# Performance work log

Measured on AMD Instinct MI355X. Metric: run time of the kernel, lower is better.

Reference implementation:

```python
import jax, jax.numpy as jnp
import numpy as np

B, N, F = 32, 1024, 32
EPS = 1e-5


def _bn(h):
    # torch BatchNorm1d(x.size(1)) applied to [B, N, C]: normalizes each node index
    # over (batch, channel) axes, training mode, biased variance, weight=1, bias=0.
    m = h.mean(axis=(0, 2), keepdims=True)
    v = h.var(axis=(0, 2), keepdims=True)
    return (h - m) / jnp.sqrt(v + EPS)


def setup_inputs() -> dict:
    key = jax.random.key(0)
    ks = jax.random.split(key, 16)
    x = jax.random.normal(ks[0], (B, N, F), dtype=jnp.float32)
    adj = jax.random.uniform(ks[1], (B, N, N), dtype=jnp.float32)

    def w(k, i, o):
        return jax.random.normal(k, (i, o), dtype=jnp.float32) * (1.0 / np.sqrt(i))

    inp = {
        'x': x, 'adj': adj,
        'W1': w(ks[2], F, 4), 'b1': jnp.zeros((4,), jnp.float32),
        'W2': w(ks[3], 4, 2), 'b2': jnp.zeros((2,), jnp.float32),
        'W3': w(ks[4], 6, 4), 'b3': jnp.zeros((4,), jnp.float32),
        'W5': w(ks[5], 6, 4), 'b5': jnp.zeros((4,), jnp.float32),
        'W7': w(ks[6], 6, 4), 'b7': jnp.zeros((4,), jnp.float32),
        'Wl': w(ks[7], 24, 3), 'bl': jnp.zeros((3,), jnp.float32),
    }
    return inp


def reference(x, adj, W1, b1, W2, b2, W3, b3, W5, b5, W7, b7, Wl, bl):
    n = adj.shape[-1]
    # DenseGCNConv normalization (identical for every conv call): set diag to 1,
    # then D^{-1/2} A D^{-1/2} with degree clamped at 1. Precompute once.
    diag = jnp.eye(n, dtype=bool)
    A = jnp.where(diag, jnp.asarray(1.0, adj.dtype), adj)  # [B,N,N]
    d = jnp.clip(A.sum(-1), 1.0, None) ** -0.5              # [B,N]
    A = d[:, :, None] * A * d[:, None, :]

    def gcn(h, W, b):
        return jnp.matmul(A, jnp.matmul(h, W)) + b

    def block(h, Wa, ba):
        x1 = _bn(jax.nn.relu(gcn(h, Wa, ba)))      # [B,N,4]
        x2 = _bn(jax.nn.relu(gcn(x1, W2, b2)))     # [B,N,2] (conv2 reused)
        x12 = jnp.concatenate([x1, x2], axis=-1)   # [B,N,6]
        return x12, x12.max(axis=1)                # pooled [B,6]

    h, p1 = block(x, W1, b1)
    h, p2 = block(h, W3, b3)
    h, p3 = block(h, W5, b5)
    h, p4 = block(h, W7, b7)
    out = jnp.concatenate([p1, p2, p3, p4], axis=-1)  # [B,24]
    ypred = out @ Wl + bl                             # [B,3]
    return ypred
```

## Files before the change

### kernel.cpp

```cpp
#include <hip/hip_runtime.h>
#include <hip/hip_fp16.h>

#define NB 32
#define NN 1024

typedef _Float16 h2 __attribute__((ext_vector_type(2)));
typedef _Float16 h8 __attribute__((ext_vector_type(8)));

static const size_t F_D     = 0;
static const size_t F_STATS = 32768;
static const size_t F_XW1   = 49152;
static constexpr size_t F_Y[8] = {180224, 311296, 376832, 507904,
                                  573440, 704512, 770048, 901120};
static const size_t AH_BYTE_OFF  = 3866624;
static const size_t WS_NEED_HALF = AH_BYTE_OFF + (size_t)NB*NN*NN*2;

__device__ __forceinline__ float fdot2f(h2 a, h2 b, float c) {
#if __has_builtin(__builtin_amdgcn_fdot2)
    return __builtin_amdgcn_fdot2(a, b, c, false);
#else
    return c + (float)a[0]*(float)b[0] + (float)a[1]*(float)b[1];
#endif
}

__global__ __launch_bounds__(256)
void k0_prep(const float* __restrict__ adj, const float* __restrict__ x,
             const float* __restrict__ W1, float* __restrict__ dd,
             float* __restrict__ xw1, float* __restrict__ stats,
             __half* __restrict__ ahw)
{
    const int tid = threadIdx.x;
    const int bx  = blockIdx.x;
    if (bx < 8192) {
        const int lane = tid & 63, wid = tid >> 6;
        const int row = bx * 4 + wid;
        const int n = row & (NN - 1);
        const float4* arow = (const float4*)(adj + (size_t)row * NN);
        uint2* hrow = (uint2*)(ahw + (size_t)row * NN);
        float s = 0.f;
        #pragma unroll
        for (int it = 0; it < 4; ++it) {
            const int idx = lane + it * 64;
            float4 v = arow[idx];
            const int k0 = idx * 4;
            v.x = (k0 + 0 == n) ? 1.f : v.x;
            v.y = (k0 + 1 == n) ? 1.f : v.y;
            v.z = (k0 + 2 == n) ? 1.f : v.z;
            v.w = (k0 + 3 == n) ? 1.f : v.w;
            s += v.x + v.y + v.z + v.w;
            if (ahw) {
                __half2 h01 = __floats2half2_rn(v.x, v.y);
                __half2 h23 = __floats2half2_rn(v.z, v.w);
                uint2 u;
                u.x = *(unsigned*)&h01; u.y = *(unsigned*)&h23;
                hrow[idx] = u;
            }
        }
        #pragma unroll
        for (int m = 1; m < 64; m <<= 1) s += __shfl_xor(s, m);
        if (lane == 0) dd[row] = rsqrtf(fmaxf(s, 1.f));
    } else if (bx < 8320) {
        const int id = (bx - 8192) * 256 + tid;
        const float4* xr = (const float4*)(x + (size_t)id * 32);
        float in[32];
        #pragma unroll
        for (int i = 0; i < 8; ++i) {
            float4 v = xr[i];
            in[4*i]=v.x; in[4*i+1]=v.y; in[4*i+2]=v.z; in[4*i+3]=v.w;
        }
        float o[4] = {0.f,0.f,0.f,0.f};
        #pragma unroll
        for (int i = 0; i < 32; ++i)
            #pragma unroll
            for (int c = 0; c < 4; ++c) o[c] += in[i] * W1[i*4+c];
        *(float4*)(xw1 + (size_t)id * 4) = make_float4(o[0],o[1],o[2],o[3]);
    } else {
        const int id = (bx - 8320) * 256 + tid;
        stats[id] = 0.f;
    }
}

__device__ __forceinline__ void stage_chunk(const __half* __restrict__ ah,
        int rowbase, int wid, int lane, int ck, char* sbuf)
{
    #pragma unroll
    for (int i = 0; i < 4; ++i) {
        const int ob = (wid << 12) + (i << 10);
        const int o  = ob + (lane << 4);
        const int row = o >> 9;
        const int scol = (o & 511) ^ ((row & 7) << 4);
        const char* g = (const char*)ah +
            (((size_t)(rowbase + row)) * NN + (size_t)ck * 256) * 2 + scol;
#if __has_builtin(__builtin_amdgcn_global_load_lds)
        __builtin_amdgcn_global_load_lds(
            (const __attribute__((address_space(1))) void*)g,
            (__attribute__((address_space(3))) void*)(sbuf + ob),
            16, 0, 0);
#else
        *(float4*)(sbuf + o) = *(const float4*)g;
#endif
    }
}

template<int CIN1, int CIN2, int COUT>
__global__ __launch_bounds__(512, 4)
void pass_half(const __half* __restrict__ ah, const float* __restrict__ dd,
               const float* __restrict__ xw1,
               const float* __restrict__ src1, const float* __restrict__ st1,
               const float* __restrict__ src2, const float* __restrict__ st2,
               const float* __restrict__ W, const float* __restrict__ bias,
               float* __restrict__ Y, float* __restrict__ stout)
{
    __shared__ char sA[2][32768];
    __shared__ _Float16 XPh[COUT][1280];
    const int tid = threadIdx.x, lane = tid & 63, wid = tid >> 6;
    const int b    = blockIdx.x >> 4;
    const int tile = (blockIdx.x & 15) << 6;
    const int rowbase = b * NN + tile;

    stage_chunk(ah, rowbase, wid, lane, 0, sA[0]);

    for (int k = tid; k < NN; k += 512) {
        float xw[COUT];
        if constexpr (CIN1 == 0) {
            const float4 v = *(const float4*)(xw1 + ((size_t)b*NN + k) * 4);
            xw[0]=v.x; xw[1]=v.y; xw[2]=v.z; xw[3]=v.w;
        } else {
            float in[CIN1 + CIN2];
            {
                const float cnt = 1.f / (32.f * CIN1);
                const float m  = st1[k] * cnt;
                const float ms = st1[NN + k] * cnt;
                const float iv = rsqrtf(ms - m*m + 1e-5f);
                const float4 v = *(const float4*)(src1 + ((size_t)b*NN + k) * CIN1);
                in[0]=(v.x-m)*iv; in[1]=(v.y-m)*iv; in[2]=(v.z-m)*iv; in[3]=(v.w-m)*iv;
            }
            if constexpr (CIN2 > 0) {
                const float cnt = 1.f / (32.f * CIN2);
                const float m  = st2[k] * cnt;
                const float ms = st2[NN + k] * cnt;
                const float iv = rsqrtf(ms - m*m + 1e-5f);
                const float2 v = *(const float2*)(src2 + ((size_t)b*NN + k) * CIN2);
                in[CIN1+0]=(v.x-m)*iv; in[CIN1+1]=(v.y-m)*iv;
            }
            #pragma unroll
            for (int c = 0; c < COUT; ++c) {
                float s = 0.f;
                #pragma unroll
                for (int i = 0; i < CIN1+CIN2; ++i) s += in[i]*W[i*COUT+c];
                xw[c] = s;
            }
        }
        const float dk = dd[b*NN + k];
        const int mk = k + ((k>>5)<<3);
        #pragma unroll
        for (int c = 0; c < COUT; ++c) XPh[c][mk] = (_Float16)(xw[c]*dk);
    }
    asm volatile("s_waitcnt vmcnt(0)" ::: "memory");
    __syncthreads();

    const int rj = lane >> 3, ll = lane & 7;
    const int trow = (wid << 3) + rj;
    float acc[COUT];
    #pragma unroll
    for (int c = 0; c < COUT; ++c) acc[c] = 0.f;

    int buf = 0;
    for (int ck = 0; ck < 4; ++ck) {
        if (ck < 3) stage_chunk(ah, rowbase, wid, lane, ck+1, sA[buf^1]);
        const char* aB = &sA[buf][trow << 9];
        #pragma unroll
        for (int sub = 0; sub < 4; ++sub) {
            const h8 av = *(const h8*)(aB + (((((ll<<2)+sub)) ^ rj) << 4));
            const int k = ck*256 + ll*32 + sub*8;
            const int mk = k + ((k>>5)<<3);
            #pragma unroll
            for (int c = 0; c < COUT; ++c) {
                const h8 xv = *(const h8*)&XPh[c][mk];
                float s = acc[c];
                s = fdot2f(h2{av[0],av[1]}, h2{xv[0],xv[1]}, s);
                s = fdot2f(h2{av[2],av[3]}, h2{xv[2],xv[3]}, s);
                s = fdot2f(h2{av[4],av[5]}, h2{xv[4],xv[5]}, s);
                s = fdot2f(h2{av[6],av[7]}, h2{xv[6],xv[7]}, s);
                acc[c] = s;
            }
        }
        asm volatile("s_waitcnt vmcnt(0)" ::: "memory");
        __syncthreads();
        buf ^= 1;
    }

    #pragma unroll
    for (int c = 0; c < COUT; ++c) {
        float v = acc[c];
        v += __shfl_xor(v, 1); v += __shfl_xor(v, 2); v += __shfl_xor(v, 4);
        acc[c] = v;
    }
    if (ll == 0) {
        const int n = tile + trow;
        const float dn = dd[b*NN + n];
        float s = 0.f, q2 = 0.f;
        float y[COUT];
        #pragma unroll
        for (int c = 0; c < COUT; ++c) {
            float t = acc[c] * dn + bias[c];
            t = fmaxf(t, 0.f);
            y[c] = t; s += t; q2 += t*t;
        }
        if constexpr (COUT == 4)
            *(float4*)(Y + ((size_t)(b*NN + n))*4) = make_float4(y[0],y[1],y[2],y[3]);
        else
            *(float2*)(Y + ((size_t)(b*NN + n))*2) = make_float2(y[0],y[1]);
        atomicAdd(stout + n, s);
        atomicAdd(stout + NN + n, q2);
    }
}

template<int CIN1, int CIN2, int COUT>
__global__ __launch_bounds__(512)
void pass_f32(const float* __restrict__ adj, const float* __restrict__ dd,
              const float* __restrict__ xw1,
              const float* __restrict__ src1, const float* __restrict__ st1,
              const float* __restrict__ src2, const float* __restrict__ st2,
              const float* __restrict__ W, const float* __restrict__ bias,
              float* __restrict__ Y, float* __restrict__ stout)
{
    __shared__ float XP[COUT][NN + (NN/32)*4];
    const int tid  = threadIdx.x;
    const int b    = blockIdx.x >> 5;
    const int tile = (blockIdx.x & 31) * 32;

    for (int k = tid; k < NN; k += 512) {
        float xw[COUT];
        if constexpr (CIN1 == 0) {
            const float4 v = *(const float4*)(xw1 + ((size_t)b*NN + k) * 4);
            xw[0]=v.x; xw[1]=v.y; xw[2]=v.z; xw[3]=v.w;
        } else {
            float in[CIN1 + CIN2];
            {
                const float cnt = 1.f / (32.f * CIN1);
                float m  = st1[k] * cnt;
                float ms = st1[NN + k] * cnt;
                float iv = rsqrtf(ms - m*m + 1e-5f);
                const float4 v = *(const float4*)(src1 + ((size_t)b*NN + k) * CIN1);
                in[0]=(v.x-m)*iv; in[1]=(v.y-m)*iv; in[2]=(v.z-m)*iv; in[3]=(v.w-m)*iv;
            }
            if constexpr (CIN2 > 0) {
                const float cnt = 1.f / (32.f * CIN2);
                float m  = st2[k] * cnt;
                float ms = st2[NN + k] * cnt;
                float iv = rsqrtf(ms - m*m + 1e-5f);
                const float2 v = *(const float2*)(src2 + ((size_t)b*NN + k) * CIN2);
                in[CIN1+0]=(v.x-m)*iv; in[CIN1+1]=(v.y-m)*iv;
            }
            #pragma unroll
            for (int c = 0; c < COUT; ++c) {
                float s = 0.f;
                #pragma unroll
                for (int i = 0; i < CIN1+CIN2; ++i) s += in[i]*W[i*COUT+c];
                xw[c] = s;
            }
        }
        const float dk = dd[(size_t)b*NN + k];
        const int mk = k + ((k >> 5) << 2);
        #pragma unroll
        for (int c = 0; c < COUT; ++c) XP[c][mk] = xw[c]*dk;
    }
    __syncthreads();

    const int lane = tid & 63, wid = tid >> 6;
    const int r0 = tile + wid * 4;
    float acc[4][COUT];
    #pragma unroll
    for (int j = 0; j < 4; ++j)
        #pragma unroll
        for (int c = 0; c < COUT; ++c) acc[j][c] = 0.f;
    float dn[4]; size_t rb[4];
    #pragma unroll
    for (int j = 0; j < 4; ++j) {
        dn[j] = dd[(size_t)b*NN + r0 + j];
        rb[j] = ((size_t)(b*NN + r0 + j)) * NN;
    }
    #pragma unroll
    for (int it = 0; it < 4; ++it) {
        const int kw = 4 * (lane + 64 * it);
        const int mb = kw + ((kw >> 5) << 2);
        float xwv[COUT][4];
        #pragma unroll
        for (int c = 0; c < COUT; ++c) {
            const float4 v = *(const float4*)&XP[c][mb];
            xwv[c][0]=v.x; xwv[c][1]=v.y; xwv[c][2]=v.z; xwv[c][3]=v.w;
        }
        #pragma unroll
        for (int j = 0; j < 4; ++j) {
            const int rr = r0 + j;
            float4 a = *(const float4*)(adj + rb[j] + kw);
            a.x = (kw + 0 == rr) ? 1.f : a.x;
            a.y = (kw + 1 == rr) ? 1.f : a.y;
            a.z = (kw + 2 == rr) ? 1.f : a.z;
            a.w = (kw + 3 == rr) ? 1.f : a.w;
            #pragma unroll
            for (int c = 0; c < COUT; ++c) {
                float s = acc[j][c];
                s = fmaf(a.x, xwv[c][0], s); s = fmaf(a.y, xwv[c][1], s);
                s = fmaf(a.z, xwv[c][2], s); s = fmaf(a.w, xwv[c][3], s);
                acc[j][c] = s;
            }
        }
    }
    #pragma unroll
    for (int j = 0; j < 4; ++j) {
        #pragma unroll
        for (int c = 0; c < COUT; ++c) {
            float v = acc[j][c];
            #pragma unroll
            for (int m = 1; m < 64; m <<= 1) v += __shfl_xor(v, m);
            acc[j][c] = v;
        }
        if (lane == 0) {
            float s = 0.f, q = 0.f;
            #pragma unroll
            for (int c = 0; c < COUT; ++c) {
                float y = acc[j][c] * dn[j] + bias[c];
                y = fmaxf(y, 0.f);
                Y[((size_t)(b*NN + r0 + j)) * COUT + c] = y;
                s += y; q += y * y;
            }
            atomicAdd(stout + (r0 + j), s);
            atomicAdd(stout + NN + (r0 + j), q);
        }
    }
}

__global__ __launch_bounds__(256)
void k_final(const float* __restrict__ Y1, const float* __restrict__ Y2,
             const float* __restrict__ Y3, const float* __restrict__ Y4,
             const float* __restrict__ Y5, const float* __restrict__ Y6,
             const float* __restrict__ Y7, const float* __restrict__ Y8,
             const float* __restrict__ stats,
             const float* __restrict__ Wl, const float* __restrict__ bl,
             float* __restrict__ out)
{
    const float* Ya[4] = {Y1, Y3, Y5, Y7};
    const float* Yb[4] = {Y2, Y4, Y6, Y8};
    const int b = blockIdx.x, tid = threadIdx.x;
    float mx[24];
    #pragma unroll
    for (int i = 0; i < 24; ++i) mx[i] = -3.4e38f;

    for (int n = tid; n < NN; n += 256) {
        #pragma unroll
        for (int g = 0; g < 4; ++g) {
            {
                const float* st = stats + (size_t)(2*g) * 2048;
                const float cnt = 1.f / 128.f;
                float m  = st[n] * cnt;
                float ms = st[NN + n] * cnt;
                float iv = rsqrtf(ms - m*m + 1e-5f);
                const float4 v = *(const float4*)(Ya[g] + ((size_t)b*NN + n) * 4);
                mx[g*6+0] = fmaxf(mx[g*6+0], (v.x - m) * iv);
                mx[g*6+1] = fmaxf(mx[g*6+1], (v.y - m) * iv);
                mx[g*6+2] = fmaxf(mx[g*6+2], (v.z - m) * iv);
                mx[g*6+3] = fmaxf(mx[g*6+3], (v.w - m) * iv);
            }
            {
                const float* st = stats + (size_t)(2*g+1) * 2048;
                const float cnt = 1.f / 64.f;
                float m  = st[n] * cnt;
                float ms = st[NN + n] * cnt;
                float iv = rsqrtf(ms - m*m + 1e-5f);
                const float2 v = *(const float2*)(Yb[g] + ((size_t)b*NN + n) * 2);
                mx[g*6+4] = fmaxf(mx[g*6+4], (v.x - m) * iv);
                mx[g*6+5] = fmaxf(mx[g*6+5], (v.y - m) * iv);
            }
        }
    }
    const int lane = tid & 63, wid = tid >> 6;
    #pragma unroll
    for (int i = 0; i < 24; ++i) {
        float v = mx[i];
        #pragma unroll
        for (int m = 1; m < 64; m <<= 1) v = fmaxf(v, __shfl_xor(v, m));
        mx[i] = v;
    }
    __shared__ float red[4][24];
    __shared__ float pooled[24];
    if (lane == 0) {
        #pragma unroll
        for (int i = 0; i < 24; ++i) red[wid][i] = mx[i];
    }
    __syncthreads();
    if (tid < 24)
        pooled[tid] = fmaxf(fmaxf(red[0][tid], red[1][tid]),
                            fmaxf(red[2][tid], red[3][tid]));
    __syncthreads();
    if (tid < 3) {
        float s = bl[tid];
        #pragma unroll
        for (int c = 0; c < 24; ++c) s += pooled[c] * Wl[c*3 + tid];
        out[b*3 + tid] = s;
    }
}

extern "C" void kernel_launch(void* const* d_in, const int* in_sizes, int n_in,
                              void* d_out, int out_size, void* d_ws, size_t ws_size,
                              hipStream_t stream)
{
    const float* x   = (const float*)d_in[0];
    const float* adj = (const float*)d_in[1];
    const float* W1  = (const float*)d_in[2];
    const float* b1  = (const float*)d_in[3];
    const float* W2  = (const float*)d_in[4];
    const float* b2  = (const float*)d_in[5];
    const float* W3  = (const float*)d_in[6];
    const float* b3  = (const float*)d_in[7];
    const float* W5  = (const float*)d_in[8];
    const float* b5  = (const float*)d_in[9];
    const float* W7  = (const float*)d_in[10];
    const float* b7  = (const float*)d_in[11];
    const float* Wl  = (const float*)d_in[12];
    const float* bl  = (const float*)d_in[13];
    float* out = (float*)d_out;

    float* wsf   = (float*)d_ws;
    float* dd    = wsf + F_D;
    float* stats = wsf + F_STATS;
    float* xw1   = wsf + F_XW1;
    float* Y[8];
    #pragma unroll
    for (int i = 0; i < 8; ++i) Y[i] = wsf + F_Y[i];
    __half* ah = (__half*)((char*)d_ws + AH_BYTE_OFF);
    const bool use_half = (ws_size >= WS_NEED_HALF);

    k0_prep<<<8384, 256, 0, stream>>>(adj, x, W1, dd, xw1, stats,
                                      use_half ? ah : nullptr);

    #define STT(i) (stats + (i)*2048)
    if (use_half) {
        const dim3 pg(512), pb(512);
        pass_half<0,0,4><<<pg, pb, 0, stream>>>(ah, dd, xw1,
            nullptr, nullptr, nullptr, nullptr, nullptr, b1, Y[0], STT(0));
        pass_half<4,0,2><<<pg, pb, 0, stream>>>(ah, dd, nullptr,
            Y[0], STT(0), nullptr, nullptr, W2, b2, Y[1], STT(1));
        pass_half<4,2,4><<<pg, pb, 0, stream>>>(ah, dd, nullptr,
            Y[0], STT(0), Y[1], STT(1), W3, b3, Y[2], STT(2));
        pass_half<4,0,2><<<pg, pb, 0, stream>>>(ah, dd, nullptr,
            Y[2], STT(2), nullptr, nullptr, W2, b2, Y[3], STT(3));
        pass_half<4,2,4><<<pg, pb, 0, stream>>>(ah, dd, nullptr,
            Y[2], STT(2), Y[3], STT(3), W5, b5, Y[4], STT(4));
        pass_half<4,0,2><<<pg, pb, 0, stream>>>(ah, dd, nullptr,
            Y[4], STT(4), nullptr, nullptr, W2, b2, Y[5], STT(5));
        pass_half<4,2,4><<<pg, pb, 0, stream>>>(ah, dd, nullptr,
            Y[4], STT(4), Y[5], STT(5), W7, b7, Y[6], STT(6));
        pass_half<4,0,2><<<pg, pb, 0, stream>>>(ah, dd, nullptr,
            Y[6], STT(6), nullptr, nullptr, W2, b2, Y[7], STT(7));
    } else {
        const dim3 pg(1024), pb(512);
        pass_f32<0,0,4><<<pg, pb, 0, stream>>>(adj, dd, xw1,
            nullptr, nullptr, nullptr, nullptr, nullptr, b1, Y[0], STT(0));
        pass_f32<4,0,2><<<pg, pb, 0, stream>>>(adj, dd, nullptr,
            Y[0], STT(0), nullptr, nullptr, W2, b2, Y[1], STT(1));
        pass_f32<4,2,4><<<pg, pb, 0, stream>>>(adj, dd, nullptr,
            Y[0], STT(0), Y[1], STT(1), W3, b3, Y[2], STT(2));
        pass_f32<4,0,2><<<pg, pb, 0, stream>>>(adj, dd, nullptr,
            Y[2], STT(2), nullptr, nullptr, W2, b2, Y[3], STT(3));
        pass_f32<4,2,4><<<pg, pb, 0, stream>>>(adj, dd, nullptr,
            Y[2], STT(2), Y[3], STT(3), W5, b5, Y[4], STT(4));
        pass_f32<4,0,2><<<pg, pb, 0, stream>>>(adj, dd, nullptr,
            Y[4], STT(4), nullptr, nullptr, W2, b2, Y[5], STT(5));
        pass_f32<4,2,4><<<pg, pb, 0, stream>>>(adj, dd, nullptr,
            Y[4], STT(4), Y[5], STT(5), W7, b7, Y[6], STT(6));
        pass_f32<4,0,2><<<pg, pb, 0, stream>>>(adj, dd, nullptr,
            Y[6], STT(6), nullptr, nullptr, W2, b2, Y[7], STT(7));
    }
    #undef STT

    k_final<<<32, 256, 0, stream>>>(Y[0], Y[1], Y[2], Y[3], Y[4], Y[5], Y[6], Y[7],
                                    stats, Wl, bl, out);
}
```

Before: 155.7 us.

## Load fp16 adjacency rows directly into registers instead of staging through LDS

Result: slower. 182.0 us (+16.9%).

```diff
diff --git a/kernel.cpp b/kernel.cpp
--- a/kernel.cpp
+++ b/kernel.cpp
@@ -80,28 +80,6 @@
     }
 }
 
-__device__ __forceinline__ void stage_chunk(const __half* __restrict__ ah,
-        int rowbase, int wid, int lane, int ck, char* sbuf)
-{
-    #pragma unroll
-    for (int i = 0; i < 4; ++i) {
-        const int ob = (wid << 12) + (i << 10);
-        const int o  = ob + (lane << 4);
-        const int row = o >> 9;
-        const int scol = (o & 511) ^ ((row & 7) << 4);
-        const char* g = (const char*)ah +
-            (((size_t)(rowbase + row)) * NN + (size_t)ck * 256) * 2 + scol;
-#if __has_builtin(__builtin_amdgcn_global_load_lds)
-        __builtin_amdgcn_global_load_lds(
-            (const __attribute__((address_space(1))) void*)g,
-            (__attribute__((address_space(3))) void*)(sbuf + ob),
-            16, 0, 0);
-#else
-        *(float4*)(sbuf + o) = *(const float4*)g;
-#endif
-    }
-}
-
 template<int CIN1, int CIN2, int COUT>
 __global__ __launch_bounds__(512, 4)
 void pass_half(const __half* __restrict__ ah, const float* __restrict__ dd,
@@ -111,14 +89,12 @@
                const float* __restrict__ W, const float* __restrict__ bias,
                float* __restrict__ Y, float* __restrict__ stout)
 {
-    __shared__ char sA[2][32768];
-    __shared__ _Float16 XPh[COUT][1280];
+    constexpr int HG = 8*COUT + 4;
+    __shared__ _Float16 XPt[128 * HG];
     const int tid = threadIdx.x, lane = tid & 63, wid = tid >> 6;
-    const int b    = blockIdx.x >> 4;
+    const int g = lane >> 5, l32 = lane & 31;
+    const int b = blockIdx.x >> 4;
     const int tile = (blockIdx.x & 15) << 6;
-    const int rowbase = b * NN + tile;
-
-    stage_chunk(ah, rowbase, wid, lane, 0, sA[0]);
 
     for (int k = tid; k < NN; k += 512) {
         float xw[COUT];
@@ -152,67 +128,80 @@
             }
         }
         const float dk = dd[b*NN + k];
-        const int mk = k + ((k>>5)<<3);
-        #pragma unroll
-        for (int c = 0; c < COUT; ++c) XPh[c][mk] = (_Float16)(xw[c]*dk);
-    }
-    asm volatile("s_waitcnt vmcnt(0)" ::: "memory");
+        const int mbase = (k>>3)*HG + ((k>>1)&3)*(2*COUT) + (k&1);
+        #pragma unroll
+        for (int c = 0; c < COUT; ++c)
+            XPt[mbase + 2*c] = (_Float16)(xw[c]*dk);
+    }
     __syncthreads();
 
-    const int rj = lane >> 3, ll = lane & 7;
-    const int trow = (wid << 3) + rj;
-    float acc[COUT];
-    #pragma unroll
-    for (int c = 0; c < COUT; ++c) acc[c] = 0.f;
-
-    int buf = 0;
-    for (int ck = 0; ck < 4; ++ck) {
-        if (ck < 3) stage_chunk(ah, rowbase, wid, lane, ck+1, sA[buf^1]);
-        const char* aB = &sA[buf][trow << 9];
-        #pragma unroll
-        for (int sub = 0; sub < 4; ++sub) {
-            const h8 av = *(const h8*)(aB + (((((ll<<2)+sub)) ^ rj) << 4));
-            const int k = ck*256 + ll*32 + sub*8;
-            const int mk = k + ((k>>5)<<3);
-            #pragma unroll
-            for (int c = 0; c < COUT; ++c) {
-                const h8 xv = *(const h8*)&XPh[c][mk];
-                float s = acc[c];
-                s = fdot2f(h2{av[0],av[1]}, h2{xv[0],xv[1]}, s);
-                s = fdot2f(h2{av[2],av[3]}, h2{xv[2],xv[3]}, s);
-                s = fdot2f(h2{av[4],av[5]}, h2{xv[4],xv[5]}, s);
-                s = fdot2f(h2{av[6],av[7]}, h2{xv[6],xv[7]}, s);
-                acc[c] = s;
-            }
-        }
-        asm volatile("s_waitcnt vmcnt(0)" ::: "memory");
-        __syncthreads();
-        buf ^= 1;
-    }
-
-    #pragma unroll
-    for (int c = 0; c < COUT; ++c) {
-        float v = acc[c];
-        v += __shfl_xor(v, 1); v += __shfl_xor(v, 2); v += __shfl_xor(v, 4);
-        acc[c] = v;
-    }
-    if (ll == 0) {
-        const int n = tile + trow;
-        const float dn = dd[b*NN + n];
-        float s = 0.f, q2 = 0.f;
-        float y[COUT];
+    const int r0 = tile + wid*8 + g*4;
+    const __half* ab[4];
+    #pragma unroll
+    for (int j = 0; j < 4; ++j)
+        ab[j] = ah + ((size_t)(b*NN + r0 + j)) * NN;
+
+    float acc[4][COUT];
+    #pragma unroll
+    for (int j = 0; j < 4; ++j)
+        #pragma unroll
+        for (int c = 0; c < COUT; ++c) acc[j][c] = 0.f;
+
+    #pragma unroll
+    for (int it = 0; it < 4; ++it) {
+        const int k = it*256 + l32*8;
+        h8 av[4];
+        #pragma unroll
+        for (int j = 0; j < 4; ++j) av[j] = *(const h8*)(ab[j] + k);
+        const h8* xp = (const h8*)&XPt[(k>>3) * HG];
+        h8 xt[COUT];
+        #pragma unroll
+        for (int q = 0; q < COUT; ++q) xt[q] = xp[q];
+        const h2* x2 = (const h2*)&xt[0];
+        #pragma unroll
+        for (int j = 0; j < 4; ++j) {
+            const h2* a2 = (const h2*)&av[j];
+            #pragma unroll
+            for (int c = 0; c < COUT; ++c) {
+                float s = acc[j][c];
+                #pragma unroll
+                for (int p = 0; p < 4; ++p)
+                    s = fdot2f(a2[p], x2[p*COUT + c], s);
+                acc[j][c] = s;
+            }
+        }
+    }
+
+    #pragma unroll
+    for (int j = 0; j < 4; ++j)
         #pragma unroll
         for (int c = 0; c < COUT; ++c) {
-            float t = acc[c] * dn + bias[c];
-            t = fmaxf(t, 0.f);
-            y[c] = t; s += t; q2 += t*t;
-        }
-        if constexpr (COUT == 4)
-            *(float4*)(Y + ((size_t)(b*NN + n))*4) = make_float4(y[0],y[1],y[2],y[3]);
-        else
-            *(float2*)(Y + ((size_t)(b*NN + n))*2) = make_float2(y[0],y[1]);
-        atomicAdd(stout + n, s);
-        atomicAdd(stout + NN + n, q2);
+            float v = acc[j][c];
+            v += __shfl_xor(v, 1);  v += __shfl_xor(v, 2);
+            v += __shfl_xor(v, 4);  v += __shfl_xor(v, 8);
+            v += __shfl_xor(v, 16);
+            acc[j][c] = v;
+        }
+    if (l32 == 0) {
+        #pragma unroll
+        for (int j = 0; j < 4; ++j) {
+            const int n = r0 + j;
+            const float dn = dd[b*NN + n];
+            float s = 0.f, q2 = 0.f;
+            float y[COUT];
+            #pragma unroll
+            for (int c = 0; c < COUT; ++c) {
+                float t = acc[j][c] * dn + bias[c];
+                t = fmaxf(t, 0.f);
+                y[c] = t; s += t; q2 += t*t;
+            }
+            if constexpr (COUT == 4)
+                *(float4*)(Y + ((size_t)(b*NN + n))*4) = make_float4(y[0],y[1],y[2],y[3]);
+            else
+                *(float2*)(Y + ((size_t)(b*NN + n))*2) = make_float2(y[0],y[1]);
+            atomicAdd(stout + n, s);
+            atomicAdd(stout + NN + n, q2);
+        }
     }
 }
 
```
